# Kernel optimization log

Hardware: AMD Instinct MI355X
Metric: run time of the kernel (lower is better)

Reference implementation:

```python
import jax, jax.numpy as jnp
import numpy as np

DIM = 384
RES = 32
NH = 8
RD = 2
B = 64


def _linear_params(key, out_f, in_f, scale=0.02, bias=True):
    kw, kb = jax.random.split(key)
    W = jax.random.normal(kw, (out_f, in_f), dtype=jnp.float32) * scale
    b = jax.random.normal(kb, (out_f,), dtype=jnp.float32) * scale if bias else None
    return W, b


def setup_inputs() -> dict:
    key = jax.random.key(0)
    ks = jax.random.split(key, 16)
    x = jax.random.normal(ks[0], (B, RES, RES, DIM), dtype=jnp.float32)
    Wc_h, bc_h = _linear_params(ks[1], NH * RD, DIM)
    Wg_h, bg_h = _linear_params(ks[2], RES * RES, RES * RD)
    Wo_h, bo_h = _linear_params(ks[3], DIM, DIM)
    Wc_w, bc_w = _linear_params(ks[4], NH * RD, DIM)
    Wg_w, bg_w = _linear_params(ks[5], RES * RES, RES * RD)
    Wo_w, bo_w = _linear_params(ks[6], DIM, DIM)
    Wmlpc, _ = _linear_params(ks[7], DIM, DIM, bias=False)
    Wr1, br1 = _linear_params(ks[8], DIM // 4, DIM)
    Wr2, br2 = _linear_params(ks[9], DIM * 3, DIM // 4)
    Wp, bp = _linear_params(ks[10], DIM, DIM)
    return dict(x=x, Wc_h=Wc_h, bc_h=bc_h, Wg_h=Wg_h, bg_h=bg_h, Wo_h=Wo_h, bo_h=bo_h,
                Wc_w=Wc_w, bc_w=bc_w, Wg_w=Wg_w, bg_w=bg_w, Wo_w=Wo_w, bo_w=bo_w,
                Wmlpc=Wmlpc, Wr1=Wr1, br1=br1, Wr2=Wr2, br2=br2, Wp=Wp, bp=bp)


def _dynamixer_op(x, Wc, bc, Wg, bg, Wo, bo):
    # x: [N, L, C]
    N, L, C = x.shape
    hd = C // NH
    # compress -> [N, L, NH*RD] -> [N, NH, L*RD]
    w = x @ Wc.T + bc
    w = w.reshape(N, L, NH, RD).transpose(0, 2, 1, 3).reshape(N, NH, L * RD)
    # generate -> [N, NH, L, L], softmax over axis -2 (rows)
    w = (w @ Wg.T + bg).reshape(N, NH, L, L)
    w = jax.nn.softmax(w, axis=-2)
    # x -> [N, NH, hd, L]; mix: y[n,h,d,j] = sum_l x[n,h,d,l] * w[n,h,l,j]
    xh = x.reshape(N, L, NH, hd).transpose(0, 2, 3, 1)
    y = jnp.einsum('nhdl,nhlj->nhdj', xh, w)
    y = y.transpose(0, 3, 1, 2).reshape(N, L, C)
    return y @ Wo.T + bo


def reference(x, Wc_h, bc_h, Wg_h, bg_h, Wo_h, bo_h,
              Wc_w, bc_w, Wg_w, bg_w, Wo_w, bo_w,
              Wmlpc, Wr1, br1, Wr2, br2, Wp, bp):
    Bn, H, W, C = x.shape
    # mix along H: batch over (B, W)
    h = _dynamixer_op(x.transpose(0, 2, 1, 3).reshape(Bn * W, H, C),
                      Wc_h, bc_h, Wg_h, bg_h, Wo_h, bo_h)
    h = h.reshape(Bn, W, H, C).transpose(0, 2, 1, 3)
    # mix along W: batch over (B, H)
    w = _dynamixer_op(x.reshape(Bn * H, W, C),
                      Wc_w, bc_w, Wg_w, bg_w, Wo_w, bo_w)
    w = w.reshape(Bn, H, W, C)
    # channel path (no bias)
    c = x @ Wmlpc.T
    # reweighting: global average pool over H, W
    a = (h + w + c).mean(axis=(1, 2))            # [B, C]
    a = jax.nn.gelu(a @ Wr1.T + br1, approximate=False) @ Wr2.T + br2  # [B, 3C]
    a = a.reshape(Bn, C, 3).transpose(2, 0, 1)   # [3, B, C]
    a = jax.nn.softmax(a, axis=0)[:, :, None, None, :]  # [3, B, 1, 1, C]
    out = h * a[0] + w * a[1] + c * a[2]
    return out @ Wp.T + bp
```

## Files before the change

kernel.cpp:

```cpp
#include <hip/hip_runtime.h>

typedef unsigned short u16;
typedef __bf16 bf16_t;
typedef bf16_t bf16x8 __attribute__((ext_vector_type(8)));
typedef float f32x4 __attribute__((ext_vector_type(4)));

__device__ __forceinline__ u16 f2b(float f) {
  union { float f; unsigned u; } v; v.f = f;
  unsigned r = (v.u + 0x7fffu + ((v.u >> 16) & 1u)) >> 16;
  return (u16)r;
}
__device__ __forceinline__ float b2f(u16 b) {
  union { unsigned u; float f; } v; v.u = ((unsigned)b) << 16;
  return v.f;
}
__device__ __forceinline__ f32x4 mfma16(bf16x8 a, bf16x8 b, f32x4 c) {
  return __builtin_amdgcn_mfma_f32_16x16x32_bf16(a, b, c, 0, 0, 0);
}

struct CvtJobs {
  const float* s[8];
  u16* d[8];
  int n[8];
};
__global__ void k0_cvt(CvtJobs j) {
  int job = blockIdx.y;
  const float* s = j.s[job];
  u16* d = j.d[job];
  int n = j.n[job];
  int stride = gridDim.x * blockDim.x * 4;
  for (int i = (blockIdx.x * blockDim.x + threadIdx.x) * 4; i < n; i += stride) {
    float4 v = *(const float4*)(s + i);
    ushort4 o4;
    o4.x = f2b(v.x); o4.y = f2b(v.y); o4.z = f2b(v.z); o4.w = f2b(v.w);
    *(ushort4*)(d + i) = o4;
  }
}

#define LW 392
#define TW 40
#define AW 40

__global__ __launch_bounds__(256, 2) void k1_mixer(
    const float* __restrict__ x,
    const u16* __restrict__ Wc_h_b, const float* __restrict__ bc_h,
    const u16* __restrict__ Wg_h_b, const float* __restrict__ bg_h,
    const u16* __restrict__ Wc_w_b, const float* __restrict__ bc_w,
    const u16* __restrict__ Wg_w_b, const float* __restrict__ bg_w,
    u16* __restrict__ y_h,
    float* __restrict__ psum_yh, float* __restrict__ psum_yw,
    float* __restrict__ psum_x)
{
  __shared__ u16 xs_b[32 * LW];
  __shared__ u16 xs_t[384 * TW];
  __shared__ u16 attn[8 * 32 * AW];
  __shared__ u16 whead[16 * 72];
  __shared__ float rs[8 * 32];

  const int tid = threadIdx.x;
  const int bid = blockIdx.x;
  const int path = bid >> 11;
  const int n = bid & 2047;
  const int b = n >> 5, o = n & 31;
  long base; int strideL;
  if (path == 0) { base = (long)b * 393216 + (long)o * 384;   strideL = 12288; }
  else           { base = (long)b * 393216 + (long)o * 12288; strideL = 384; }
  const float* xseq = x + base;

  const u16* Wc_b = path ? Wc_w_b : Wc_h_b;
  const float* bc = path ? bc_w : bc_h;
  const u16* Wg_b = path ? Wg_w_b : Wg_h_b;
  const float* bg = path ? bg_w : bg_h;

  for (int i = tid; i < 3072; i += 256) {
    int l = i / 96, c4 = (i % 96) * 4;
    float4 v = *(const float4*)(xseq + (long)l * strideL + c4);
    ushort4 w4;
    w4.x = f2b(v.x); w4.y = f2b(v.y); w4.z = f2b(v.z); w4.w = f2b(v.w);
    *(ushort4*)&xs_b[l * LW + c4] = w4;
  }
  for (int i = tid; i < 576; i += 256) whead[576 + i] = 0;
  __syncthreads();

  if (path == 0) {
    for (int i = tid; i < 3072; i += 256) {
      int c = i % 384, l4 = (i / 384) * 4;
      ushort4 w4;
      w4.x = xs_b[(l4 + 0) * LW + c];
      w4.y = xs_b[(l4 + 1) * LW + c];
      w4.z = xs_b[(l4 + 2) * LW + c];
      w4.w = xs_b[(l4 + 3) * LW + c];
      *(ushort4*)&xs_t[c * TW + l4] = w4;
    }
    for (int c = tid; c < 384; c += 256) {
      float s = 0.f;
      for (int l = 0; l < 32; l++) s += b2f(xs_b[l * LW + c]);
      psum_x[(long)n * 384 + c] = s;
    }
  }

  const int wave = tid >> 6, lane = tid & 63;
  const int lq = lane >> 4, lr = lane & 15;
  const f32x4 z = {0.f, 0.f, 0.f, 0.f};

  if (wave < 2) {
    f32x4 acc = z;
    for (int ks = 0; ks < 12; ks++) {
      bf16x8 af  = *(const bf16x8*)&xs_b[(wave * 16 + lr) * LW + ks * 32 + lq * 8];
      bf16x8 bfr = *(const bf16x8*)(Wc_b + lr * 384 + ks * 32 + lq * 8);
      acc = mfma16(af, bfr, acc);
    }
    float bcv = bc[lr];
    for (int r = 0; r < 4; r++) {
      int l = wave * 16 + lq * 4 + r;
      whead[(lr >> 1) * 72 + l * 2 + (lr & 1)] = f2b(acc[r] + bcv);
    }
  }
  __syncthreads();

  {
    bf16x8 ga0 = *(const bf16x8*)&whead[lr * 72 + lq * 8];
    bf16x8 ga1 = *(const bf16x8*)&whead[lr * 72 + 32 + lq * 8];
    for (int t = 0; t < 16; t++) {
      int nt = wave * 16 + t;
      const u16* wg = Wg_b + (nt * 16 + lr) * 64;
      bf16x8 gb0 = *(const bf16x8*)(wg + lq * 8);
      bf16x8 gb1 = *(const bf16x8*)(wg + 32 + lq * 8);
      f32x4 acc = z;
      acc = mfma16(ga0, gb0, acc);
      acc = mfma16(ga1, gb1, acc);
      if (lq < 2) {
        int m = nt * 16 + lr, ii = m >> 5, jj = m & 31;
        for (int r = 0; r < 4; r++)
          attn[((lq * 4 + r) * 32 + jj) * AW + ii] = f2b(acc[r]);
      }
    }
  }
  __syncthreads();

  {
    int h = tid >> 5, j = tid & 31;
    u16* row = &attn[(h * 32 + j) * AW];
    float v[32]; float mx = -1e30f;
    for (int i = 0; i < 32; i++) {
      v[i] = b2f(row[i]) + bg[i * 32 + j];
      mx = fmaxf(mx, v[i]);
    }
    float s = 0.f;
    for (int i = 0; i < 32; i++) { v[i] = __expf(v[i] - mx); s += v[i]; }
    float inv = 1.0f / s;
    for (int i = 0; i < 32; i++) row[i] = f2b(v[i] * inv);
  }
  __syncthreads();

  if (path == 0) {
    for (int hh = 0; hh < 2; hh++) {
      int h = wave * 2 + hh;
      bf16x8 bf0 = *(const bf16x8*)&attn[(h * 32 + lr) * AW + lq * 8];
      bf16x8 bf1 = *(const bf16x8*)&attn[(h * 32 + 16 + lr) * AW + lq * 8];
      for (int mt = 0; mt < 3; mt++) {
        bf16x8 af = *(const bf16x8*)&xs_t[(h * 48 + mt * 16 + lr) * TW + lq * 8];
        f32x4 a0 = mfma16(af, bf0, z);
        f32x4 a1 = mfma16(af, bf1, z);
        for (int r = 0; r < 4; r++) {
          int c = h * 48 + mt * 16 + lq * 4 + r;
          xs_b[lr * LW + c]        = f2b(a0[r]);
          xs_b[(16 + lr) * LW + c] = f2b(a1[r]);
        }
      }
    }
    __syncthreads();
    u16* yout = y_h + base;
    for (int i = tid; i < 1536; i += 256) {
      int l = i / 48, uu = (i % 48) * 8;
      *(uint4*)(yout + (long)l * strideL + uu) = *(const uint4*)&xs_b[l * LW + uu];
    }
    for (int c = tid; c < 384; c += 256) {
      float s = 0.f;
      for (int jj = 0; jj < 32; jj++) s += b2f(xs_b[jj * LW + c]);
      psum_yh[(long)n * 384 + c] = s;
    }
  } else {
    {
      int h = tid >> 5, l = tid & 31;
      float s = 0.f;
      for (int j = 0; j < 32; j++) s += b2f(attn[(h * 32 + j) * AW + l]);
      rs[h * 32 + l] = s;
    }
    __syncthreads();
    for (int c = tid; c < 384; c += 256) {
      int h = c / 48;
      float s = 0.f;
      for (int l = 0; l < 32; l++) s += b2f(xs_b[l * LW + c]) * rs[h * 32 + l];
      psum_yw[(long)n * 384 + c] = s;
    }
  }
}

__global__ __launch_bounds__(384) void k3_scales(
    const float* __restrict__ psum_yh, const float* __restrict__ psum_yw,
    const float* __restrict__ psum_x,
    const float* __restrict__ Wo_h, const float* __restrict__ bo_h,
    const float* __restrict__ Wo_w, const float* __restrict__ bo_w,
    const float* __restrict__ Wmlpc,
    const float* __restrict__ Wr1, const float* __restrict__ br1,
    const float* __restrict__ Wr2, const float* __restrict__ br2,
    float* __restrict__ scal)
{
  __shared__ float ph[384], pw[384], px[384], a[384], r1[96];
  int b = blockIdx.x, t = threadIdx.x;
  float sh = 0.f, sw = 0.f, sx = 0.f;
  for (int o = 0; o < 32; o++) {
    sh += psum_yh[(long)(b * 32 + o) * 384 + t];
    sw += psum_yw[(long)(b * 32 + o) * 384 + t];
    sx += psum_x[(long)(b * 32 + o) * 384 + t];
  }
  ph[t] = sh; pw[t] = sw; px[t] = sx;
  __syncthreads();
  float s1 = 0.f, s2 = 0.f, s3 = 0.f;
  for (int k = 0; k < 384; k++) {
    s1 += ph[k] * Wo_h[t * 384 + k];
    s2 += pw[k] * Wo_w[t * 384 + k];
    s3 += px[k] * Wmlpc[t * 384 + k];
  }
  a[t] = (s1 + s2 + s3) * (1.f / 1024.f) + bo_h[t] + bo_w[t];
  __syncthreads();
  if (t < 96) {
    float s = 0.f;
    for (int k = 0; k < 384; k++) s += a[k] * Wr1[t * 384 + k];
    s += br1[t];
    r1[t] = s * 0.5f * (1.f + erff(s * 0.70710678118654752f));
  }
  __syncthreads();
  {
    float sv[3];
    for (int si = 0; si < 3; si++) {
      float acc = 0.f;
      for (int k = 0; k < 96; k++) acc += r1[k] * Wr2[(t * 3 + si) * 96 + k];
      sv[si] = acc + br2[t * 3 + si];
    }
    float mx = fmaxf(sv[0], fmaxf(sv[1], sv[2]));
    float e0 = __expf(sv[0] - mx), e1 = __expf(sv[1] - mx), e2 = __expf(sv[2] - mx);
    float inv = 1.f / (e0 + e1 + e2);
    scal[0 * 24576 + b * 384 + t] = e0 * inv;
    scal[1 * 24576 + b * 384 + t] = e1 * inv;
    scal[2 * 24576 + b * 384 + t] = e2 * inv;
  }
}

__device__ __forceinline__ void gemm_acc(
    const u16* __restrict__ Bglob, const float* __restrict__ sc,
    const u16* bufA, u16* Bs, f32x4 acc[4][6],
    int wm, int wn, int lq, int lr, int tid)
{
  for (int ks = 0; ks < 12; ks++) {
    for (int i = tid; i < 1536; i += 512) {
      int row = i >> 2, k8 = (i & 3) * 8;
      const u16* g = Bglob + row * 384 + ks * 32 + k8;
      if (sc) {
        float s = sc[row];
        alignas(16) u16 tmp[8];
        for (int u = 0; u < 8; u++) tmp[u] = f2b(b2f(g[u]) * s);
        *(uint4*)&Bs[row * 40 + k8] = *(const uint4*)tmp;
      } else {
        *(uint4*)&Bs[row * 40 + k8] = *(const uint4*)g;
      }
    }
    __syncthreads();
    bf16x8 af[4];
    for (int mt = 0; mt < 4; mt++)
      af[mt] = *(const bf16x8*)&bufA[(wm * 64 + mt * 16 + lr) * 392 + ks * 32 + lq * 8];
    for (int nt = 0; nt < 6; nt++) {
      bf16x8 bfr = *(const bf16x8*)&Bs[(wn * 96 + nt * 16 + lr) * 40 + lq * 8];
      for (int mt = 0; mt < 4; mt++)
        acc[mt][nt] = mfma16(af[mt], bfr, acc[mt][nt]);
    }
    __syncthreads();
  }
}

__global__ __launch_bounds__(512, 2) void k24_final(
    const float* __restrict__ x, const u16* __restrict__ y_h,
    const u16* __restrict__ Wc_w_b, const float* __restrict__ bc_w,
    const u16* __restrict__ Wg_w_b, const float* __restrict__ bg_w,
    const u16* __restrict__ Wo_h_b, const u16* __restrict__ Wo_w_b,
    const u16* __restrict__ Wmlpc_b, const u16* __restrict__ Wp_b,
    const float* __restrict__ bo_h, const float* __restrict__ bo_w,
    const float* __restrict__ bp,
    const float* __restrict__ scal, float* __restrict__ out)
{
  __shared__ u16 bufA[128 * 392];
  __shared__ u16 Bs[384 * 40];
  __shared__ u16 attn[8 * 32 * AW];
  __shared__ u16 whead[16 * 72];

  const int tid = threadIdx.x;
  const int m0 = blockIdx.x * 128;
  const int b = m0 >> 10;
  const int wave = tid >> 6, lane = tid & 63;
  const int lq = lane >> 4, lr = lane & 15;
  const int wm = wave >> 2, wn = wave & 3;
  const f32x4 z = {0.f, 0.f, 0.f, 0.f};

  for (int i = tid; i < 12288; i += 512) {
    int row = i / 96, c4 = (i % 96) * 4;
    float4 v = *(const float4*)(x + (long)(m0 + row) * 384 + c4);
    ushort4 w4;
    w4.x = f2b(v.x); w4.y = f2b(v.y); w4.z = f2b(v.z); w4.w = f2b(v.w);
    *(ushort4*)&bufA[row * 392 + c4] = w4;
  }
  for (int i = tid; i < 576; i += 512) whead[576 + i] = 0;
  __syncthreads();

  f32x4 acc[4][6];
  for (int i = 0; i < 4; i++)
    for (int jn = 0; jn < 6; jn++) acc[i][jn] = z;

  gemm_acc(Wmlpc_b, scal + 2 * 24576 + b * 384, bufA, Bs, acc, wm, wn, lq, lr, tid);

  for (int q = 0; q < 4; q++) {
    for (int i = tid; i < 3072; i += 512) {
      int c = i % 384, l4 = (i / 384) * 4;
      ushort4 w4;
      w4.x = bufA[(q * 32 + l4 + 0) * 392 + c];
      w4.y = bufA[(q * 32 + l4 + 1) * 392 + c];
      w4.z = bufA[(q * 32 + l4 + 2) * 392 + c];
      w4.w = bufA[(q * 32 + l4 + 3) * 392 + c];
      *(ushort4*)&Bs[c * 40 + l4] = w4;
    }
    if (wave < 2) {
      f32x4 ac = z;
      for (int ks = 0; ks < 12; ks++) {
        bf16x8 afg = *(const bf16x8*)&bufA[(q * 32 + wave * 16 + lr) * 392 + ks * 32 + lq * 8];
        bf16x8 bfg = *(const bf16x8*)(Wc_w_b + lr * 384 + ks * 32 + lq * 8);
        ac = mfma16(afg, bfg, ac);
      }
      float bcv = bc_w[lr];
      for (int r = 0; r < 4; r++) {
        int l = wave * 16 + lq * 4 + r;
        whead[(lr >> 1) * 72 + l * 2 + (lr & 1)] = f2b(ac[r] + bcv);
      }
    }
    __syncthreads();
    {
      bf16x8 ga0 = *(const bf16x8*)&whead[lr * 72 + lq * 8];
      bf16x8 ga1 = *(const bf16x8*)&whead[lr * 72 + 32 + lq * 8];
      for (int t = 0; t < 8; t++) {
        int nt = wave * 8 + t;
        const u16* wg = Wg_w_b + (nt * 16 + lr) * 64;
        bf16x8 gb0 = *(const bf16x8*)(wg + lq * 8);
        bf16x8 gb1 = *(const bf16x8*)(wg + 32 + lq * 8);
        f32x4 ac = z;
        ac = mfma16(ga0, gb0, ac);
        ac = mfma16(ga1, gb1, ac);
        if (lq < 2) {
          int m = nt * 16 + lr, ii = m >> 5, jj = m & 31;
          for (int r = 0; r < 4; r++)
            attn[((lq * 4 + r) * 32 + jj) * AW + ii] = f2b(ac[r]);
        }
      }
    }
    __syncthreads();
    if (tid < 256) {
      int h = tid >> 5, j = tid & 31;
      u16* row = &attn[(h * 32 + j) * AW];
      float v[32]; float mx = -1e30f;
      for (int i = 0; i < 32; i++) {
        v[i] = b2f(row[i]) + bg_w[i * 32 + j];
        mx = fmaxf(mx, v[i]);
      }
      float s = 0.f;
      for (int i = 0; i < 32; i++) { v[i] = __expf(v[i] - mx); s += v[i]; }
      float inv = 1.0f / s;
      for (int i = 0; i < 32; i++) row[i] = f2b(v[i] * inv);
    }
    __syncthreads();
    {
      int h = wave;
      bf16x8 bf0 = *(const bf16x8*)&attn[(h * 32 + lr) * AW + lq * 8];
      bf16x8 bf1 = *(const bf16x8*)&attn[(h * 32 + 16 + lr) * AW + lq * 8];
      for (int mt = 0; mt < 3; mt++) {
        bf16x8 afg = *(const bf16x8*)&Bs[(h * 48 + mt * 16 + lr) * 40 + lq * 8];
        f32x4 a0 = mfma16(afg, bf0, z);
        f32x4 a1 = mfma16(afg, bf1, z);
        for (int r = 0; r < 4; r++) {
          int c = h * 48 + mt * 16 + lq * 4 + r;
          bufA[(q * 32 + lr) * 392 + c]      = f2b(a0[r]);
          bufA[(q * 32 + 16 + lr) * 392 + c] = f2b(a1[r]);
        }
      }
    }
    __syncthreads();
  }

  gemm_acc(Wo_w_b, scal + 1 * 24576 + b * 384, bufA, Bs, acc, wm, wn, lq, lr, tid);

  for (int i = tid; i < 6144; i += 512) {
    int row = i / 48, u8 = (i % 48) * 8;
    *(uint4*)&bufA[row * 392 + u8] = *(const uint4*)(y_h + (long)(m0 + row) * 384 + u8);
  }
  __syncthreads();
  gemm_acc(Wo_h_b, scal + 0 * 24576 + b * 384, bufA, Bs, acc, wm, wn, lq, lr, tid);

  for (int nt = 0; nt < 6; nt++) {
    int col = wn * 96 + nt * 16 + lr;
    float bcb = scal[b * 384 + col] * bo_h[col] +
                scal[24576 + b * 384 + col] * bo_w[col];
    for (int mt = 0; mt < 4; mt++)
      for (int r = 0; r < 4; r++) {
        int row = wm * 64 + mt * 16 + lq * 4 + r;
        bufA[row * 392 + col] = f2b(acc[mt][nt][r] + bcb);
      }
  }
  __syncthreads();

  for (int i = 0; i < 4; i++)
    for (int jn = 0; jn < 6; jn++) acc[i][jn] = z;
  gemm_acc(Wp_b, nullptr, bufA, Bs, acc, wm, wn, lq, lr, tid);
  for (int nt = 0; nt < 6; nt++) {
    int col = wn * 96 + nt * 16 + lr;
    float bi = bp[col];
    for (int mt = 0; mt < 4; mt++)
      for (int r = 0; r < 4; r++) {
        int row = m0 + wm * 64 + mt * 16 + lq * 4 + r;
        out[(long)row * 384 + col] = acc[mt][nt][r] + bi;
      }
  }
}

extern "C" void kernel_launch(void* const* d_in, const int* in_sizes, int n_in,
                              void* d_out, int out_size, void* d_ws, size_t ws_size,
                              hipStream_t stream) {
  const float* x     = (const float*)d_in[0];
  const float* Wc_h  = (const float*)d_in[1];
  const float* bc_h  = (const float*)d_in[2];
  const float* Wg_h  = (const float*)d_in[3];
  const float* bg_h  = (const float*)d_in[4];
  const float* Wo_h  = (const float*)d_in[5];
  const float* bo_h  = (const float*)d_in[6];
  const float* Wc_w  = (const float*)d_in[7];
  const float* bc_w  = (const float*)d_in[8];
  const float* Wg_w  = (const float*)d_in[9];
  const float* bg_w  = (const float*)d_in[10];
  const float* Wo_w  = (const float*)d_in[11];
  const float* bo_w  = (const float*)d_in[12];
  const float* Wmlpc = (const float*)d_in[13];
  const float* Wr1   = (const float*)d_in[14];
  const float* br1   = (const float*)d_in[15];
  const float* Wr2   = (const float*)d_in[16];
  const float* br2   = (const float*)d_in[17];
  const float* Wp    = (const float*)d_in[18];
  const float* bp    = (const float*)d_in[19];
  float* out = (float*)d_out;

  char* ws = (char*)d_ws;
  u16* y_h       = (u16*)(ws + 0);
  float* psum_yh = (float*)(ws + 50331648);
  float* psum_yw = (float*)(ws + 53477376);
  float* psum_x  = (float*)(ws + 56623104);
  float* scal    = (float*)(ws + 59768832);
  u16* Wc_h_b    = (u16*)(ws + 60063744);
  u16* Wc_w_b    = (u16*)(ws + 60076032);
  u16* Wg_h_b    = (u16*)(ws + 60088320);
  u16* Wg_w_b    = (u16*)(ws + 60219392);
  u16* Wo_h_b    = (u16*)(ws + 60350464);
  u16* Wo_w_b    = (u16*)(ws + 60645376);
  u16* Wmlpc_b   = (u16*)(ws + 60940288);
  u16* Wp_b      = (u16*)(ws + 61235200);

  CvtJobs jobs;
  jobs.s[0] = Wc_h;  jobs.d[0] = Wc_h_b;  jobs.n[0] = 6144;
  jobs.s[1] = Wc_w;  jobs.d[1] = Wc_w_b;  jobs.n[1] = 6144;
  jobs.s[2] = Wg_h;  jobs.d[2] = Wg_h_b;  jobs.n[2] = 65536;
  jobs.s[3] = Wg_w;  jobs.d[3] = Wg_w_b;  jobs.n[3] = 65536;
  jobs.s[4] = Wo_h;  jobs.d[4] = Wo_h_b;  jobs.n[4] = 147456;
  jobs.s[5] = Wo_w;  jobs.d[5] = Wo_w_b;  jobs.n[5] = 147456;
  jobs.s[6] = Wmlpc; jobs.d[6] = Wmlpc_b; jobs.n[6] = 147456;
  jobs.s[7] = Wp;    jobs.d[7] = Wp_b;    jobs.n[7] = 147456;
  k0_cvt<<<dim3(144, 8), 256, 0, stream>>>(jobs);

  k1_mixer<<<4096, 256, 0, stream>>>(x, Wc_h_b, bc_h, Wg_h_b, bg_h,
      Wc_w_b, bc_w, Wg_w_b, bg_w, y_h, psum_yh, psum_yw, psum_x);

  k3_scales<<<64, 384, 0, stream>>>(psum_yh, psum_yw, psum_x, Wo_h, bo_h,
      Wo_w, bo_w, Wmlpc, Wr1, br1, Wr2, br2, scal);

  k24_final<<<512, 512, 0, stream>>>(x, y_h, Wc_w_b, bc_w, Wg_w_b, bg_w,
      Wo_h_b, Wo_w_b, Wmlpc_b, Wp_b, bo_h, bo_w, bp, scal, out);
}
```

Baseline: 663.1 us.

## Load GEMM B fragments directly into registers and fold scales into accumulators

Replaces the LDS-staged B-tile GEMM, which had per-k-step syncthreads and per-element rescaling of weights by the softmax scales, with direct global-to-register fragment loads that are software-prefetched one k-step ahead. The per-branch scaling is moved onto the accumulators by multiplying them by ratios of consecutive scales, with a final multiply by the last scale. This removes LDS traffic, barriers and scalar bf16 conversions from the inner loop. In exchange it adds register pressure, relies on uncoalesced-ish global or L2 weight reads, and divides by scales clamped at 1e-30, which changes rounding slightly.

```diff
diff --git a/kernel.cpp b/kernel.cpp
--- a/kernel.cpp
+++ b/kernel.cpp
@@ -248,34 +248,33 @@
   }
 }
 
-__device__ __forceinline__ void gemm_acc(
-    const u16* __restrict__ Bglob, const float* __restrict__ sc,
-    const u16* bufA, u16* Bs, f32x4 acc[4][6],
-    int wm, int wn, int lq, int lr, int tid)
+__device__ __forceinline__ void gemm_regB(
+    const u16* __restrict__ Bglob, const u16* __restrict__ bufA,
+    f32x4 acc[4][6], int wm, int wn, int lq, int lr)
 {
+  const u16* bp0 = Bglob + (wn * 96 + lr) * 384 + lq * 8;
+  const u16* ap0 = bufA + (wm * 64 + lr) * 392 + lq * 8;
+  bf16x8 bcur[6], af[4];
+#pragma unroll
+  for (int nt = 0; nt < 6; nt++) bcur[nt] = *(const bf16x8*)(bp0 + nt * 6144);
+#pragma unroll
+  for (int mt = 0; mt < 4; mt++) af[mt] = *(const bf16x8*)(ap0 + mt * 6272);
   for (int ks = 0; ks < 12; ks++) {
-    for (int i = tid; i < 1536; i += 512) {
-      int row = i >> 2, k8 = (i & 3) * 8;
-      const u16* g = Bglob + row * 384 + ks * 32 + k8;
-      if (sc) {
-        float s = sc[row];
-        alignas(16) u16 tmp[8];
-        for (int u = 0; u < 8; u++) tmp[u] = f2b(b2f(g[u]) * s);
-        *(uint4*)&Bs[row * 40 + k8] = *(const uint4*)tmp;
-      } else {
-        *(uint4*)&Bs[row * 40 + k8] = *(const uint4*)g;
-      }
-    }
-    __syncthreads();
-    bf16x8 af[4];
-    for (int mt = 0; mt < 4; mt++)
-      af[mt] = *(const bf16x8*)&bufA[(wm * 64 + mt * 16 + lr) * 392 + ks * 32 + lq * 8];
-    for (int nt = 0; nt < 6; nt++) {
-      bf16x8 bfr = *(const bf16x8*)&Bs[(wn * 96 + nt * 16 + lr) * 40 + lq * 8];
+    bf16x8 bnx[6], an[4];
+    const int k1 = (ks < 11) ? (ks + 1) * 32 : 11 * 32;
+#pragma unroll
+    for (int nt = 0; nt < 6; nt++) bnx[nt] = *(const bf16x8*)(bp0 + nt * 6144 + k1);
+#pragma unroll
+    for (int mt = 0; mt < 4; mt++) an[mt] = *(const bf16x8*)(ap0 + mt * 6272 + k1);
+#pragma unroll
+    for (int nt = 0; nt < 6; nt++)
+#pragma unroll
       for (int mt = 0; mt < 4; mt++)
-        acc[mt][nt] = mfma16(af[mt], bfr, acc[mt][nt]);
-    }
-    __syncthreads();
+        acc[mt][nt] = mfma16(af[mt], bcur[nt], acc[mt][nt]);
+#pragma unroll
+    for (int nt = 0; nt < 6; nt++) bcur[nt] = bnx[nt];
+#pragma unroll
+    for (int mt = 0; mt < 4; mt++) af[mt] = an[mt];
   }
 }
 
@@ -313,10 +312,26 @@
   __syncthreads();
 
   f32x4 acc[4][6];
+#pragma unroll
   for (int i = 0; i < 4; i++)
+#pragma unroll
     for (int jn = 0; jn < 6; jn++) acc[i][jn] = z;
 
-  gemm_acc(Wmlpc_b, scal + 2 * 24576 + b * 384, bufA, Bs, acc, wm, wn, lq, lr, tid);
+  gemm_regB(Wmlpc_b, bufA, acc, wm, wn, lq, lr);
+
+  {
+    const float* s2p = scal + 2 * 24576 + b * 384;
+    const float* s1p = scal + 1 * 24576 + b * 384;
+#pragma unroll
+    for (int nt = 0; nt < 6; nt++) {
+      int col = wn * 96 + nt * 16 + lr;
+      float r = s2p[col] / fmaxf(s1p[col], 1e-30f);
+#pragma unroll
+      for (int mt = 0; mt < 4; mt++)
+#pragma unroll
+        for (int rr = 0; rr < 4; rr++) acc[mt][nt][rr] *= r;
+    }
+  }
 
   for (int q = 0; q < 4; q++) {
     for (int i = tid; i < 3072; i += 512) {
@@ -393,34 +408,64 @@
     __syncthreads();
   }
 
-  gemm_acc(Wo_w_b, scal + 1 * 24576 + b * 384, bufA, Bs, acc, wm, wn, lq, lr, tid);
+  gemm_regB(Wo_w_b, bufA, acc, wm, wn, lq, lr);
+
+  {
+    const float* s1p = scal + 1 * 24576 + b * 384;
+    const float* s0p = scal + 0 * 24576 + b * 384;
+#pragma unroll
+    for (int nt = 0; nt < 6; nt++) {
+      int col = wn * 96 + nt * 16 + lr;
+      float r = s1p[col] / fmaxf(s0p[col], 1e-30f);
+#pragma unroll
+      for (int mt = 0; mt < 4; mt++)
+#pragma unroll
+        for (int rr = 0; rr < 4; rr++) acc[mt][nt][rr] *= r;
+    }
+  }
+
+  __syncthreads();
 
   for (int i = tid; i < 6144; i += 512) {
     int row = i / 48, u8 = (i % 48) * 8;
     *(uint4*)&bufA[row * 392 + u8] = *(const uint4*)(y_h + (long)(m0 + row) * 384 + u8);
   }
   __syncthreads();
-  gemm_acc(Wo_h_b, scal + 0 * 24576 + b * 384, bufA, Bs, acc, wm, wn, lq, lr, tid);
-
-  for (int nt = 0; nt < 6; nt++) {
-    int col = wn * 96 + nt * 16 + lr;
-    float bcb = scal[b * 384 + col] * bo_h[col] +
-                scal[24576 + b * 384 + col] * bo_w[col];
-    for (int mt = 0; mt < 4; mt++)
-      for (int r = 0; r < 4; r++) {
-        int row = wm * 64 + mt * 16 + lq * 4 + r;
-        bufA[row * 392 + col] = f2b(acc[mt][nt][r] + bcb);
-      }
-  }
-  __syncthreads();
-
+  gemm_regB(Wo_h_b, bufA, acc, wm, wn, lq, lr);
+
+  __syncthreads();
+
+  {
+    const float* s0p = scal + 0 * 24576 + b * 384;
+    const float* s1p = scal + 1 * 24576 + b * 384;
+#pragma unroll
+    for (int nt = 0; nt < 6; nt++) {
+      int col = wn * 96 + nt * 16 + lr;
+      float s0v = s0p[col];
+      float bcb = s0v * bo_h[col] + s1p[col] * bo_w[col];
+#pragma unroll
+      for (int mt = 0; mt < 4; mt++)
+#pragma unroll
+        for (int r = 0; r < 4; r++) {
+          int row = wm * 64 + mt * 16 + lq * 4 + r;
+          bufA[row * 392 + col] = f2b(acc[mt][nt][r] * s0v + bcb);
+        }
+    }
+  }
+  __syncthreads();
+
+#pragma unroll
   for (int i = 0; i < 4; i++)
+#pragma unroll
     for (int jn = 0; jn < 6; jn++) acc[i][jn] = z;
-  gemm_acc(Wp_b, nullptr, bufA, Bs, acc, wm, wn, lq, lr, tid);
+  gemm_regB(Wp_b, bufA, acc, wm, wn, lq, lr);
+#pragma unroll
   for (int nt = 0; nt < 6; nt++) {
     int col = wn * 96 + nt * 16 + lr;
     float bi = bp[col];
+#pragma unroll
     for (int mt = 0; mt < 4; mt++)
+#pragma unroll
       for (int r = 0; r < 4; r++) {
         int row = m0 + wm * 64 + mt * 16 + lq * 4 + r;
         out[(long)row * 384 + col] = acc[mt][nt][r] + bi;
```

Result: faster. 647.4 us (-2.4%).
